# Optimization experiments

Hardware: AMD Instinct MI355X
Metric: run time of the kernel (lower is better)

Reference implementation:

```python
import jax, jax.numpy as jnp
import numpy as np

# Module constants (from init_kwargs / derived)
KH, KW = 3, 3
STRIDE = (1, 1)
PAD = (1, 1)
DIL = (1, 1)
N_OFFSET_GRPS = 8  # offset.shape[1] // (2*KH*KW) = 144 // 18
N_WEIGHT_GRPS = 1


def setup_inputs() -> dict:
    key = jax.random.key(0)
    k1, k2, k3, k4, k5 = jax.random.split(key, 5)
    B, C, H, W = 4, 64, 128, 128
    inp = {
        "input": jax.random.normal(k1, (B, C, H, W), dtype=jnp.float32),
        "offset": jax.random.normal(k2, (B, 2 * N_OFFSET_GRPS * KH * KW, H, W), dtype=jnp.float32),
        "mask": jax.random.uniform(k3, (B, N_OFFSET_GRPS * KH * KW, H, W), dtype=jnp.float32),
        "weight": jax.random.normal(k4, (64, C, KH, KW), dtype=jnp.float32) * 0.05,
        "bias": jax.random.normal(k5, (64,), dtype=jnp.float32) * 0.05,
    }
    return inp


def _deform_conv2d(x, offset, mask, weight, bias):
    B, C, H, W = x.shape
    Ho, Wo = offset.shape[2], offset.shape[3]
    G = N_OFFSET_GRPS
    K = KH * KW
    Cg = C // G

    # base (un-deformed) sampling positions per kernel tap and output pixel
    ky, kx = jnp.meshgrid(jnp.arange(KH), jnp.arange(KW), indexing="ij")
    ky = ky.reshape(K)
    kx = kx.reshape(K)
    oy = jnp.arange(Ho) * STRIDE[0] - PAD[0]
    ox = jnp.arange(Wo) * STRIDE[1] - PAD[1]
    base_y = (oy[None, :, None] + (ky * DIL[0])[:, None, None]).astype(x.dtype)  # [K,Ho,1]
    base_x = (ox[None, None, :] + (kx * DIL[1])[:, None, None]).astype(x.dtype)  # [K,1,Wo]

    off = offset.reshape(B, G, K, 2, Ho, Wo)  # [...,0]=dy, [...,1]=dx
    py = base_y[None, None] + off[:, :, :, 0]  # [B,G,K,Ho,Wo]
    px = base_x[None, None] + off[:, :, :, 1]

    y0 = jnp.floor(py)
    x0 = jnp.floor(px)
    ly = py - y0  # fractional parts
    lx = px - x0
    y0i = y0.astype(jnp.int32)
    x0i = x0.astype(jnp.int32)

    xg = x.reshape(B, G, Cg, H * W)  # per-offset-group channel slices

    def corner(yi, xi):
        valid = ((yi >= 0) & (yi < H) & (xi >= 0) & (xi < W)).astype(x.dtype)
        idx = jnp.clip(yi, 0, H - 1) * W + jnp.clip(xi, 0, W - 1)  # [B,G,K,Ho,Wo]
        gather = lambda xbg, ibg: xbg[:, ibg]  # [Cg,H*W],[K,Ho,Wo] -> [Cg,K,Ho,Wo]
        v = jax.vmap(jax.vmap(gather))(xg, idx)  # [B,G,Cg,K,Ho,Wo]
        return v * valid[:, :, None]

    w00 = (1 - ly) * (1 - lx)
    w01 = (1 - ly) * lx
    w10 = ly * (1 - lx)
    w11 = ly * lx
    samp = (corner(y0i, x0i) * w00[:, :, None]
            + corner(y0i, x0i + 1) * w01[:, :, None]
            + corner(y0i + 1, x0i) * w10[:, :, None]
            + corner(y0i + 1, x0i + 1) * w11[:, :, None])  # [B,G,Cg,K,Ho,Wo]

    samp = samp * mask.reshape(B, G, 1, K, Ho, Wo)  # DCNv2 modulation
    col = samp.reshape(B, C, K, Ho, Wo)
    wr = weight.reshape(weight.shape[0], C, K)  # groups == 1
    out = jnp.einsum("ock,bckhw->bohw", wr, col) + bias[None, :, None, None]
    return out


def reference(input, offset, mask, weight, bias):
    return _deform_conv2d(input, offset, mask, weight, bias)
```

## Files before the change

### kernel.cpp

```cpp
#include <hip/hip_runtime.h>

#define HH 128
#define WW 128
#define CC 64
#define CO 64
#define BB 4
#define GG 8
#define CG 8
#define KK 9
#define HW (HH*WW)
#define PXT 64

typedef __attribute__((ext_vector_type(8))) short short8;
typedef __attribute__((ext_vector_type(4))) float floatx4;
typedef __attribute__((ext_vector_type(2))) float f32x2;

union S8I { short8 s; int i[4]; };
union FU { float f; unsigned u; };

__device__ inline short f2bf(float f) {
    FU v; v.f = f;
    return (short)((v.u + 0x7FFF + ((v.u >> 16) & 1)) >> 16);
}
__device__ inline unsigned rnd2(float f) {
    FU v; v.f = f;
    return v.u + 0x8000u;
}
__device__ inline float bflo(int e) { union { int i; float f; } u; u.i = e << 16; return u.f; }
__device__ inline float bfhi(int e) { union { int i; float f; } u; u.i = e & 0xffff0000; return u.f; }

__global__ __launch_bounds__(256)
void prep(const float* __restrict__ wt, const float* __restrict__ in,
          short* __restrict__ wf, short* __restrict__ in_t) {
    const int bid = blockIdx.x;
    if (bid < 144) {
        const int tid = bid * 256 + threadIdx.x;
        const int j   = tid & 7;
        const int L   = (tid >> 3) & 63;
        const int fid = tid >> 9;
        const int ot  = fid & 3;
        const int gch = fid >> 2;
        const int h   = gch / 9, gc = gch - h * 9;
        const int o   = ot * 16 + (L & 15);
        const int g   = h * 4 + (L >> 4);
        wf[tid] = f2bf(wt[o * 576 + (g * 8 + j) * 9 + gc]);
    } else {
        const int idx = bid - 144;
        const int bx = idx & 63;
        const int g  = (idx >> 6) & 7;
        const int b  = idx >> 9;
        const int p  = bx * 256 + threadIdx.x;
        const float* src = in + (b * CC + g * CG) * HW + p;
        short8 v;
        #pragma unroll
        for (int cg = 0; cg < CG; ++cg) v[cg] = f2bf(src[cg * HW]);
        *(short8*)(in_t + ((b * GG + g) * HW + p) * 8) = v;
    }
}

__global__ __launch_bounds__(256, 4)
void dcn_fused(const short* __restrict__ in_t, const float* __restrict__ off,
               const float* __restrict__ msk, const short* __restrict__ wf,
               const float* __restrict__ bias, float* __restrict__ out)
{
    __shared__ short s_col[9 * 4 * 512];

    const int pxbase = blockIdx.x * PXT;
    const int ho = blockIdx.y;
    const int b  = blockIdx.z;
    const int t  = threadIdx.x;
    const int w = t >> 6, lane = t & 63;
    const int px = pxbase + lane;
    const int q4 = lane >> 4, n16 = lane & 15;
    const int basepix = ho * WW + px;

    floatx4 acc[4];
    #pragma unroll
    for (int ot = 0; ot < 4; ++ot)
        #pragma unroll
        for (int r = 0; r < 4; ++r)
            acc[ot][r] = bias[ot * 16 + q4 * 4 + r];

    const char* ib = (const char*)(in_t + (long)b * GG * HW * 8);

    #pragma unroll
    for (int h = 0; h < 2; ++h) {
        const int g = h * 4 + w;

        float pdy[9], pdx[9], pm[9];
        #pragma unroll
        for (int i = 0; i < 9; ++i) {
            const int offc = (b * 144 + g * 18 + i * 2) * HW + basepix;
            pdy[i] = off[offc];
            pdx[i] = off[offc + HW];
            pm[i]  = msk[(b * 72 + g * 9 + i) * HW + basepix];
        }

        if (h) __syncthreads();

        const int gsh = g << 18;
        #pragma unroll
        for (int i = 0; i < 9; ++i) {
            const int ky = i / 3, kx = i - (i / 3) * 3;

            const float py  = (float)(ho - 1 + ky) + pdy[i];
            const float pxf = (float)(px - 1 + kx) + pdx[i];
            const float y0f = floorf(py), x0f = floorf(pxf);
            const float ly = py - y0f, lx = pxf - x0f;
            const int y0 = (int)y0f, x0 = (int)x0f;
            const int y1 = y0 + 1,  x1 = x0 + 1;

            const float vy0 = (y0 >= 0 && y0 < HH) ? 1.f : 0.f;
            const float vy1 = (y1 >= 0 && y1 < HH) ? 1.f : 0.f;
            const float vx0 = (x0 >= 0 && x0 < WW) ? 1.f : 0.f;
            const float vx1 = (x1 >= 0 && x1 < WW) ? 1.f : 0.f;
            const int y0c = min(max(y0, 0), HH - 1), y1c = min(max(y1, 0), HH - 1);
            const int x0c = min(max(x0, 0), WW - 1), x1c = min(max(x1, 0), WW - 1);

            const float m = pm[i];
            const float wy0 = (1.f - ly) * vy0 * m;
            const float wy1 = ly * vy1 * m;
            const float wx0 = (1.f - lx) * vx0;
            const float wx1 = lx * vx1;
            const float w00 = wy0 * wx0, w01 = wy0 * wx1;
            const float w10 = wy1 * wx0, w11 = wy1 * wx1;

            const int y0sh = gsh + (y0c << 11), y1sh = gsh + (y1c << 11);
            const int x0sh = x0c << 4, x1sh = x1c << 4;
            S8I u00, u01, u10, u11;
            u00.s = *(const short8*)(ib + (y0sh + x0sh));
            u01.s = *(const short8*)(ib + (y0sh + x1sh));
            u10.s = *(const short8*)(ib + (y1sh + x0sh));
            u11.s = *(const short8*)(ib + (y1sh + x1sh));

            const f32x2 W00 = {w00, w00}, W01 = {w01, w01};
            const f32x2 W10 = {w10, w10}, W11 = {w11, w11};
            S8I res;
            #pragma unroll
            for (int pc = 0; pc < 4; ++pc) {
                const int e00 = u00.i[pc], e01 = u01.i[pc];
                const int e10 = u10.i[pc], e11 = u11.i[pc];
                f32x2 a00 = {bflo(e00), bfhi(e00)};
                f32x2 a01 = {bflo(e01), bfhi(e01)};
                f32x2 a10 = {bflo(e10), bfhi(e10)};
                f32x2 a11 = {bflo(e11), bfhi(e11)};
                f32x2 v = a00 * W00;
                v += a01 * W01;
                v += a10 * W10;
                v += a11 * W11;
                res.i[pc] = (int)__builtin_amdgcn_perm(rnd2(v.y), rnd2(v.x), 0x07060302u);
            }

            *(short8*)(s_col + ((i * 4 + q4) * 64 + w * 16 + n16) * 8) = res.s;
        }

        __syncthreads();

        #pragma unroll
        for (int gc = 0; gc < 9; ++gc) {
            const short8 bfr = *(const short8*)&s_col[((gc * 4 + w) * 64 + lane) * 8];
            #pragma unroll
            for (int ot = 0; ot < 4; ++ot) {
                const short8 afr = *(const short8*)&wf[((h * 9 + gc) * 4 + ot) * 512 + lane * 8];
                acc[ot] = __builtin_amdgcn_mfma_f32_16x16x32_bf16(afr, bfr, acc[ot], 0, 0, 0);
            }
        }
    }

    const int pxo = pxbase + w * 16 + n16;
    #pragma unroll
    for (int ot = 0; ot < 4; ++ot)
        #pragma unroll
        for (int r = 0; r < 4; ++r)
            out[((b * CO + ot * 16 + q4 * 4 + r) * HH + ho) * WW + pxo] = acc[ot][r];
}

extern "C" void kernel_launch(void* const* d_in, const int* in_sizes, int n_in,
                              void* d_out, int out_size, void* d_ws, size_t ws_size,
                              hipStream_t stream) {
    const float* in   = (const float*)d_in[0];
    const float* off  = (const float*)d_in[1];
    const float* msk  = (const float*)d_in[2];
    const float* wt   = (const float*)d_in[3];
    const float* bias = (const float*)d_in[4];
    float* out = (float*)d_out;
    short* wf   = (short*)d_ws;
    short* in_t = (short*)d_ws + 36864;

    prep<<<144 + 2048, 256, 0, stream>>>(wt, in, wf, in_t);

    dim3 grid(WW / PXT, HH, BB);
    dcn_fused<<<grid, 256, 0, stream>>>(in_t, off, msk, wf, bias, out);
}
```

Measured before the change: 135.4 us.

## Feed sampled bf16 values straight into MFMA B fragments, dropping shared-memory staging

Each lane now computes the bilinear sample for the pixel and offset group that match its own MFMA B-fragment position (group chosen by q4, pixel by n16 and wave). The result feeds the MFMA directly, so the shared-memory column buffer and both barriers go away. The grid is also flattened to 1D with a remapped block index, which spreads consecutive blocks across rows and batches, possibly for XCD locality. In exchange, offset and mask loads are less coalesced, since lanes in a wave now read four different groups.

```diff
diff --git a/kernel.cpp b/kernel.cpp
--- a/kernel.cpp
+++ b/kernel.cpp
@@ -63,15 +63,16 @@
                const float* __restrict__ msk, const short* __restrict__ wf,
                const float* __restrict__ bias, float* __restrict__ out)
 {
-    __shared__ short s_col[9 * 4 * 512];
+    const int lin = (blockIdx.x & 7) * 128 + (blockIdx.x >> 3);
+    const int b   = lin >> 8;
+    const int rem = lin & 255;
+    const int ho  = rem >> 1;
+    const int bx  = rem & 1;
 
-    const int pxbase = blockIdx.x * PXT;
-    const int ho = blockIdx.y;
-    const int b  = blockIdx.z;
     const int t  = threadIdx.x;
     const int w = t >> 6, lane = t & 63;
-    const int px = pxbase + lane;
     const int q4 = lane >> 4, n16 = lane & 15;
+    const int px = bx * PXT + w * 16 + n16;
     const int basepix = ho * WW + px;
 
     floatx4 acc[4];
@@ -85,7 +86,7 @@
 
     #pragma unroll
     for (int h = 0; h < 2; ++h) {
-        const int g = h * 4 + w;
+        const int g = h * 4 + q4;
 
         float pdy[9], pdx[9], pm[9];
         #pragma unroll
@@ -95,8 +96,6 @@
             pdx[i] = off[offc + HW];
             pm[i]  = msk[(b * 72 + g * 9 + i) * HW + basepix];
         }
-
-        if (h) __syncthreads();
 
         const int gsh = g << 18;
         #pragma unroll
@@ -151,28 +150,19 @@
                 res.i[pc] = (int)__builtin_amdgcn_perm(rnd2(v.y), rnd2(v.x), 0x07060302u);
             }
 
-            *(short8*)(s_col + ((i * 4 + q4) * 64 + w * 16 + n16) * 8) = res.s;
-        }
-
-        __syncthreads();
-
-        #pragma unroll
-        for (int gc = 0; gc < 9; ++gc) {
-            const short8 bfr = *(const short8*)&s_col[((gc * 4 + w) * 64 + lane) * 8];
             #pragma unroll
             for (int ot = 0; ot < 4; ++ot) {
-                const short8 afr = *(const short8*)&wf[((h * 9 + gc) * 4 + ot) * 512 + lane * 8];
-                acc[ot] = __builtin_amdgcn_mfma_f32_16x16x32_bf16(afr, bfr, acc[ot], 0, 0, 0);
+                const short8 afr = *(const short8*)&wf[((h * 9 + i) * 4 + ot) * 512 + lane * 8];
+                acc[ot] = __builtin_amdgcn_mfma_f32_16x16x32_bf16(afr, res.s, acc[ot], 0, 0, 0);
             }
         }
     }
 
-    const int pxo = pxbase + w * 16 + n16;
     #pragma unroll
     for (int ot = 0; ot < 4; ++ot)
         #pragma unroll
         for (int r = 0; r < 4; ++r)
-            out[((b * CO + ot * 16 + q4 * 4 + r) * HH + ho) * WW + pxo] = acc[ot][r];
+            out[((b * CO + ot * 16 + q4 * 4 + r) * HH + ho) * WW + px] = acc[ot][r];
 }
 
 extern "C" void kernel_launch(void* const* d_in, const int* in_sizes, int n_in,
@@ -189,6 +179,5 @@
 
     prep<<<144 + 2048, 256, 0, stream>>>(wt, in, wf, in_t);
 
-    dim3 grid(WW / PXT, HH, BB);
-    dcn_fused<<<grid, 256, 0, stream>>>(in_t, off, msk, wf, bias, out);
+    dcn_fused<<<1024, 256, 0, stream>>>(in_t, off, msk, wf, bias, out);
 }
```

After: 146.8 us. +8.4%, slower.
